# Kernel tuning notes

Measured on AMD Instinct MI355X. Metric: run time of the kernel, lower is better.

The kernel has to match this reference:

```python
import jax, jax.numpy as jnp
import numpy as np

D_MODEL = 1024
NUM_HEADS = 16
D_K = D_MODEL // NUM_HEADS


def setup_inputs() -> dict:
    key = jax.random.key(0)
    ks = jax.random.split(key, 9)
    B, S = 2, 2048
    scale = 1.0 / np.sqrt(D_MODEL)
    x = jax.random.normal(ks[0], (B, S, D_MODEL), dtype=jnp.float32)
    Wq = jax.random.normal(ks[1], (D_MODEL, D_MODEL), dtype=jnp.float32) * scale
    Wk = jax.random.normal(ks[2], (D_MODEL, D_MODEL), dtype=jnp.float32) * scale
    Wv = jax.random.normal(ks[3], (D_MODEL, D_MODEL), dtype=jnp.float32) * scale
    Wo = jax.random.normal(ks[4], (D_MODEL, D_MODEL), dtype=jnp.float32) * scale
    bq = jax.random.normal(ks[5], (D_MODEL,), dtype=jnp.float32) * 0.01
    bk = jax.random.normal(ks[6], (D_MODEL,), dtype=jnp.float32) * 0.01
    bv = jax.random.normal(ks[7], (D_MODEL,), dtype=jnp.float32) * 0.01
    bo = jax.random.normal(ks[8], (D_MODEL,), dtype=jnp.float32) * 0.01
    return {"x": x, "Wq": Wq, "bq": bq, "Wk": Wk, "bk": bk,
            "Wv": Wv, "bv": bv, "Wo": Wo, "bo": bo}


def reference(x, Wq, bq, Wk, bk, Wv, bv, Wo, bo):
    B, S, _ = x.shape
    H, Dk = NUM_HEADS, D_K
    # projections -> [B, H, S, Dk]
    def split_heads(t):
        return t.reshape(B, S, H, Dk).transpose(0, 2, 1, 3)
    q = split_heads(x @ Wq + bq)
    k = split_heads(x @ Wk + bk)
    v = split_heads(x @ Wv + bv)
    # full score matrix [B, H, S, S] (faithful to the original non-fused impl)
    scores = jnp.einsum('bhqd,bhkd->bhqk', q, k) / jnp.sqrt(jnp.float32(Dk))
    attn = jax.nn.softmax(scores, axis=-1)
    out = jnp.einsum('bhqk,bhkd->bhqd', attn, v)
    out = out.transpose(0, 2, 1, 3).reshape(B, S, H * Dk)
    return out @ Wo + bo
```

## Files before the change

### kernel.cpp

```cpp
#include <hip/hip_runtime.h>
#include <cstdint>

constexpr int S    = 2048;
constexpr int D    = 1024;
constexpr int NH   = 16;
constexpr int DK   = 64;
constexpr int MTOK = 2 * S;

typedef __bf16 bf16x8 __attribute__((ext_vector_type(8)));
typedef __bf16 bf16x4 __attribute__((ext_vector_type(4)));
typedef float  floatx4 __attribute__((ext_vector_type(4)));
typedef unsigned uintx4 __attribute__((ext_vector_type(4)));

__device__ __forceinline__ void async_cp16(const void* g, void* l) {
    __builtin_amdgcn_global_load_lds(
        (const __attribute__((address_space(1))) uint32_t*)g,
        (__attribute__((address_space(3))) uint32_t*)l, 16, 0, 0);
}

__device__ __forceinline__ void swap_rows32(unsigned &a, unsigned &b) {
#if __has_builtin(__builtin_amdgcn_permlane32_swap)
    typedef unsigned u32x2 __attribute__((ext_vector_type(2)));
    u32x2 r = __builtin_amdgcn_permlane32_swap(a, b, false, false);
    a = r[0]; b = r[1];
#else
    asm volatile("v_permlane32_swap_b32 %0, %1" : "+v"(a), "+v"(b));
#endif
}
__device__ __forceinline__ void swap_rows16(unsigned &a, unsigned &b) {
#if __has_builtin(__builtin_amdgcn_permlane16_swap)
    typedef unsigned u32x2 __attribute__((ext_vector_type(2)));
    u32x2 r = __builtin_amdgcn_permlane16_swap(a, b, false, false);
    a = r[0]; b = r[1];
#else
    asm volatile("v_permlane16_swap_b32 %0, %1" : "+v"(a), "+v"(b));
#endif
}

__global__ __launch_bounds__(256) void cvt_prep(
    const float* __restrict__ x, __bf16* __restrict__ xb,
    const float* __restrict__ W0, const float* __restrict__ W1,
    const float* __restrict__ W2, const float* __restrict__ W3,
    __bf16* __restrict__ T0, __bf16* __restrict__ T1,
    __bf16* __restrict__ T2, __bf16* __restrict__ T3)
{
    const int t = threadIdx.x;
    if (blockIdx.z == 4) {
        int blk = blockIdx.y * 16 + blockIdx.x;
        const float4* src = (const float4*)x;
        #pragma unroll
        for (int ii = 0; ii < 16; ++ii) {
            int idx = blk * 4096 + ii * 256 + t;
            float4 v = src[idx];
            bf16x4 o;
            o[0] = (__bf16)v.x; o[1] = (__bf16)v.y; o[2] = (__bf16)v.z; o[3] = (__bf16)v.w;
            *(bf16x4*)&xb[(size_t)idx * 4] = o;
        }
        return;
    }
    const float* W = (blockIdx.z == 0) ? W0 : (blockIdx.z == 1) ? W1 : (blockIdx.z == 2) ? W2 : W3;
    __bf16*      T = (blockIdx.z == 0) ? T0 : (blockIdx.z == 1) ? T1 : (blockIdx.z == 2) ? T2 : T3;
    __shared__ __bf16 tile[64][65];
    const int k0 = blockIdx.y * 64, n0 = blockIdx.x * 64;
    #pragma unroll
    for (int i = 0; i < 4; ++i) {
        int k = (t >> 4) + i * 16;
        int n = (t & 15) * 4;
        float4 v = *(const float4*)&W[(size_t)(k0 + k) * D + n0 + n];
        tile[n + 0][k] = (__bf16)v.x;
        tile[n + 1][k] = (__bf16)v.y;
        tile[n + 2][k] = (__bf16)v.z;
        tile[n + 3][k] = (__bf16)v.w;
    }
    __syncthreads();
    #pragma unroll
    for (int i = 0; i < 4; ++i) {
        int n = (t >> 4) + i * 16;
        int k = (t & 15) * 4;
        bf16x4 o;
        o[0] = tile[n][k]; o[1] = tile[n][k + 1]; o[2] = tile[n][k + 2]; o[3] = tile[n][k + 3];
        *(bf16x4*)&T[(size_t)(n0 + n) * D + k0 + k] = o;
    }
}

constexpr int BM = 128, BK = 64;

template<int JT>
__device__ __forceinline__ void gemm_core(
    const __bf16* __restrict__ A, const __bf16* __restrict__ Bt,
    __bf16* Alds, __bf16* Blds, int m0, int n0, floatx4 (&acc)[4][JT])
{
    const int tid = threadIdx.x;
    const int w = tid >> 6, l = tid & 63;
    const int wm = (w >> 1) * 64, wn = (w & 1) * 16 * JT;
    const int lr = l & 15, lg = l >> 4;

    #pragma unroll
    for (int i = 0; i < 4; ++i)
        #pragma unroll
        for (int j = 0; j < JT; ++j)
            acc[i][j] = (floatx4){0.f, 0.f, 0.f, 0.f};

    for (int k0 = 0; k0 < D; k0 += BK) {
        #pragma unroll
        for (int i = 0; i < 4; ++i) {
            int c = i * 256 + tid, row = c >> 3, g = c & 7;
            async_cp16(&A[(size_t)(m0 + row) * D + k0 + g * 8], &Alds[c * 8]);
        }
        #pragma unroll
        for (int i = 0; i < JT; ++i) {
            int c = i * 256 + tid, row = c >> 3, g = c & 7;
            async_cp16(&Bt[(size_t)(n0 + row) * D + k0 + g * 8], &Blds[c * 8]);
        }
        __syncthreads();
        #pragma unroll
        for (int kk = 0; kk < 2; ++kk) {
            bf16x8 af[4], bfr[JT];
            #pragma unroll
            for (int i = 0; i < 4; ++i)
                af[i] = *(const bf16x8*)&Alds[(wm + i * 16 + lr) * BK + kk * 32 + lg * 8];
            #pragma unroll
            for (int j = 0; j < JT; ++j)
                bfr[j] = *(const bf16x8*)&Blds[(wn + j * 16 + lr) * BK + kk * 32 + lg * 8];
            #pragma unroll
            for (int i = 0; i < 4; ++i)
                #pragma unroll
                for (int j = 0; j < JT; ++j)
                    acc[i][j] = __builtin_amdgcn_mfma_f32_16x16x32_bf16(af[i], bfr[j], acc[i][j], 0, 0, 0);
        }
        __syncthreads();
    }
}

__global__ __launch_bounds__(256, 2) void gemm_qkv(
    const __bf16* __restrict__ xb,
    const __bf16* __restrict__ WqT, const __bf16* __restrict__ WkT, const __bf16* __restrict__ WvT,
    const float* __restrict__ bq, const float* __restrict__ bk, const float* __restrict__ bv,
    __bf16* __restrict__ Qb, __bf16* __restrict__ Kb, __bf16* __restrict__ Vt)
{
    __shared__ __align__(16) __bf16 Alds[BM * BK];
    __shared__ __align__(16) __bf16 Blds[128 * BK];
    const int z = blockIdx.z;
    const __bf16* Bt   = (z == 0) ? WqT : (z == 1) ? WkT : WvT;
    const float*  bias = (z == 0) ? bq : (z == 1) ? bk : bv;
    const float   scale = (z == 0) ? 0.18033688f : 1.0f;
    const int m0 = blockIdx.y * BM, n0 = blockIdx.x * 128;

    floatx4 acc[4][4];
    gemm_core<4>(xb, Bt, Alds, Blds, m0, n0, acc);

    const int tid = threadIdx.x;
    const int w = tid >> 6, l = tid & 63;
    const int wm = (w >> 1) * 64, wn = (w & 1) * 64;
    const int lr = l & 15, lg = l >> 4;

    if (z < 2) {
        __bf16* Out = (z == 0) ? Qb : Kb;
        #pragma unroll
        for (int i = 0; i < 4; ++i)
            #pragma unroll
            for (int j = 0; j < 4; ++j) {
                int n = n0 + wn + j * 16 + lr;
                #pragma unroll
                for (int r = 0; r < 4; ++r) {
                    int m = m0 + wm + i * 16 + lg * 4 + r;
                    float v = (acc[i][j][r] + bias[n]) * scale;
                    size_t off = ((size_t)((m >> 11) * NH + (n >> 6)) * S + (m & (S - 1))) * DK + (n & (DK - 1));
                    Out[off] = (__bf16)v;
                }
            }
    } else {
        #pragma unroll
        for (int i = 0; i < 4; ++i)
            #pragma unroll
            for (int j = 0; j < 4; ++j) {
                int n = n0 + wn + j * 16 + lr;
                int m = m0 + wm + i * 16 + lg * 4;
                float bn = bias[n];
                bf16x4 o;
                #pragma unroll
                for (int r = 0; r < 4; ++r) o[r] = (__bf16)(acc[i][j][r] + bn);
                size_t off = ((size_t)((m >> 11) * NH + (n >> 6)) * DK + (n & (DK - 1))) * S + (m & (S - 1));
                *(bf16x4*)&Vt[off] = o;
            }
    }
}

__global__ __launch_bounds__(256, 2) void gemm_out(
    const __bf16* __restrict__ A, const __bf16* __restrict__ Bt,
    const float* __restrict__ bias, float* __restrict__ Cout)
{
    __shared__ __align__(16) __bf16 Alds[BM * BK];
    __shared__ __align__(16) __bf16 Blds[64 * BK];
    const int m0 = blockIdx.y * BM, n0 = blockIdx.x * 64;

    floatx4 acc[4][2];
    gemm_core<2>(A, Bt, Alds, Blds, m0, n0, acc);

    const int tid = threadIdx.x;
    const int w = tid >> 6, l = tid & 63;
    const int wm = (w >> 1) * 64, wn = (w & 1) * 32;
    const int lr = l & 15, lg = l >> 4;
    #pragma unroll
    for (int i = 0; i < 4; ++i)
        #pragma unroll
        for (int j = 0; j < 2; ++j) {
            int n = n0 + wn + j * 16 + lr;
            #pragma unroll
            for (int r = 0; r < 4; ++r) {
                int m = m0 + wm + i * 16 + lg * 4 + r;
                Cout[(size_t)m * D + n] = acc[i][j][r] + bias[n];
            }
        }
}

constexpr int QT = 128;
constexpr int KT = 64;
constexpr float SOFTMAX_C2 = 14.4269504f;

__device__ __forceinline__ unsigned pkexp(float a, float b) {
    __bf16 lo = (__bf16)__builtin_amdgcn_exp2f(a - SOFTMAX_C2);
    __bf16 hi = (__bf16)__builtin_amdgcn_exp2f(b - SOFTMAX_C2);
    unsigned ls = (unsigned)__builtin_bit_cast(unsigned short, lo);
    unsigned hs = (unsigned)__builtin_bit_cast(unsigned short, hi);
    return ls | (hs << 16);
}

__global__ __launch_bounds__(256, 2) void attn_mfma(
    const __bf16* __restrict__ Q, const __bf16* __restrict__ K,
    const __bf16* __restrict__ Vt, __bf16* __restrict__ O)
{
    __shared__ __align__(16) __bf16 Klds[2][KT * DK];
    __shared__ __align__(16) __bf16 Vlds[2][DK * KT];

    const int tid = threadIdx.x;
    const int w = tid >> 6, l = tid & 63;
    const int lr = l & 15, lg = l >> 4;
    const int sw = lr & 7;
    const int bh = blockIdx.y;
    const int q0 = blockIdx.x * QT;
    const __bf16* Kbase = K  + (size_t)bh * S * DK;
    const __bf16* Vbase = Vt + (size_t)bh * DK * S;

    bf16x8 qf[2][2];
    {
        const __bf16* qp = Q + ((size_t)bh * S + q0 + w * 32) * DK;
        #pragma unroll
        for (int i = 0; i < 2; ++i)
            #pragma unroll
            for (int kk = 0; kk < 2; ++kk)
                qf[i][kk] = *(const bf16x8*)&qp[(i * 16 + lr) * DK + kk * 32 + lg * 8];
    }
    bf16x8 vones;
    #pragma unroll
    for (int j = 0; j < 8; ++j) vones[j] = (__bf16)1.0f;

    floatx4 acc[4][2];
    #pragma unroll
    for (int jd = 0; jd < 4; ++jd)
        #pragma unroll
        for (int i = 0; i < 2; ++i)
            acc[jd][i] = (floatx4){0.f, 0.f, 0.f, 0.f};
    floatx4 psacc[2];
    psacc[0] = (floatx4){0.f, 0.f, 0.f, 0.f};
    psacc[1] = (floatx4){0.f, 0.f, 0.f, 0.f};

    bf16x8 kreg[2], vreg[2];
    auto gload = [&](int t0) {
        #pragma unroll
        for (int ii = 0; ii < 2; ++ii) {
            int c = ii * 256 + tid, row = c >> 3, g = c & 7;
            kreg[ii] = *(const bf16x8*)&Kbase[(size_t)(t0 + row) * DK + g * 8];
            vreg[ii] = *(const bf16x8*)&Vbase[(size_t)row * S + t0 + g * 8];
        }
    };
    auto lwrite = [&](int buf) {
        #pragma unroll
        for (int ii = 0; ii < 2; ++ii) {
            int c = ii * 256 + tid, row = c >> 3, gs = (c & 7) ^ (row & 7);
            *(bf16x8*)&Klds[buf][row * 64 + gs * 8] = kreg[ii];
            *(bf16x8*)&Vlds[buf][row * 64 + gs * 8] = vreg[ii];
        }
    };

    gload(0);
    lwrite(0);
    gload(KT);

    for (int t0 = 0; t0 < S; t0 += KT) {
        const int cur = (t0 >> 6) & 1;
        __syncthreads();

        floatx4 sa[4][2];
        #pragma unroll
        for (int j = 0; j < 4; ++j)
            #pragma unroll
            for (int i = 0; i < 2; ++i)
                sa[j][i] = (floatx4){0.f, 0.f, 0.f, 0.f};
        #pragma unroll
        for (int kk = 0; kk < 2; ++kk) {
            bf16x8 kf[4];
            #pragma unroll
            for (int j = 0; j < 4; ++j)
                kf[j] = *(const bf16x8*)&Klds[cur][(j * 16 + lr) * DK + (((kk * 4 + lg) ^ sw) * 8)];
            #pragma unroll
            for (int j = 0; j < 4; ++j)
                #pragma unroll
                for (int i = 0; i < 2; ++i)
                    sa[j][i] = __builtin_amdgcn_mfma_f32_16x16x32_bf16(kf[j], qf[i][kk], sa[j][i], 0, 0, 0);
        }

        bf16x8 pfr[2][2];
        #pragma unroll
        for (int i = 0; i < 2; ++i)
            #pragma unroll
            for (int kk = 0; kk < 2; ++kk) {
                const int j0 = kk * 2, j1 = j0 + 1;
                unsigned pa = pkexp(sa[j0][i][0], sa[j0][i][1]);
                unsigned pc = pkexp(sa[j0][i][2], sa[j0][i][3]);
                unsigned pb = pkexp(sa[j1][i][0], sa[j1][i][1]);
                unsigned pd = pkexp(sa[j1][i][2], sa[j1][i][3]);
                swap_rows32(pa, pb); swap_rows16(pa, pb);
                swap_rows32(pc, pd); swap_rows16(pc, pd);
                uintx4 pw = {pa, pc, pb, pd};
                pfr[kk][i] = __builtin_bit_cast(bf16x8, pw);
            }

        #pragma unroll
        for (int kk = 0; kk < 2; ++kk) {
            bf16x8 vf[4];
            #pragma unroll
            for (int jd = 0; jd < 4; ++jd)
                vf[jd] = *(const bf16x8*)&Vlds[cur][(jd * 16 + lr) * KT + (((kk * 4 + lg) ^ sw) * 8)];
            #pragma unroll
            for (int jd = 0; jd < 4; ++jd)
                #pragma unroll
                for (int i = 0; i < 2; ++i)
                    acc[jd][i] = __builtin_amdgcn_mfma_f32_16x16x32_bf16(vf[jd], pfr[kk][i], acc[jd][i], 0, 0, 0);
            #pragma unroll
            for (int i = 0; i < 2; ++i)
                psacc[i] = __builtin_amdgcn_mfma_f32_16x16x32_bf16(vones, pfr[kk][i], psacc[i], 0, 0, 0);
        }

        if (t0 + KT < S) {
            lwrite(cur ^ 1);
            if (t0 + 2 * KT < S) gload(t0 + 2 * KT);
        }
    }

    const int b = bh >> 4, h = bh & 15;
    #pragma unroll
    for (int i = 0; i < 2; ++i) {
        float inv = 1.f / psacc[i][0];
        int q = q0 + w * 32 + i * 16 + lr;
        __bf16* op = O + (size_t)(b * S + q) * D + h * DK;
        #pragma unroll
        for (int jd = 0; jd < 4; ++jd) {
            bf16x4 ov;
            #pragma unroll
            for (int r = 0; r < 4; ++r) ov[r] = (__bf16)(acc[jd][i][r] * inv);
            *(bf16x4*)&op[jd * 16 + lg * 4] = ov;
        }
    }
}

extern "C" void kernel_launch(void* const* d_in, const int* in_sizes, int n_in,
                              void* d_out, int out_size, void* d_ws, size_t ws_size,
                              hipStream_t stream) {
    const float* x  = (const float*)d_in[0];
    const float* Wq = (const float*)d_in[1];
    const float* bq = (const float*)d_in[2];
    const float* Wk = (const float*)d_in[3];
    const float* bk = (const float*)d_in[4];
    const float* Wv = (const float*)d_in[5];
    const float* bv = (const float*)d_in[6];
    const float* Wo = (const float*)d_in[7];
    const float* bo = (const float*)d_in[8];

    char* ws = (char*)d_ws;
    __bf16* xb  = (__bf16*)(ws);
    __bf16* WqT = (__bf16*)(ws + (8ull  << 20));
    __bf16* WkT = (__bf16*)(ws + (10ull << 20));
    __bf16* WvT = (__bf16*)(ws + (12ull << 20));
    __bf16* WoT = (__bf16*)(ws + (14ull << 20));
    __bf16* Qb  = (__bf16*)(ws + (16ull << 20));
    __bf16* Kb  = (__bf16*)(ws + (24ull << 20));
    __bf16* Vt  = (__bf16*)(ws + (32ull << 20));
    __bf16* Ob  = (__bf16*)(ws + (40ull << 20));

    cvt_prep<<<dim3(16, 16, 5), 256, 0, stream>>>(
        x, xb, Wq, Wk, Wv, Wo, WqT, WkT, WvT, WoT);

    gemm_qkv<<<dim3(D / 128, MTOK / BM, 3), 256, 0, stream>>>(
        xb, WqT, WkT, WvT, bq, bk, bv, Qb, Kb, Vt);

    attn_mfma<<<dim3(S / QT, 2 * NH), 256, 0, stream>>>(Qb, Kb, Vt, Ob);

    gemm_out<<<dim3(D / 64, MTOK / BM), 256, 0, stream>>>(Ob, WoT, bo, (float*)d_out);
}
```

Measured before the change: 193.9 us.

## Load K/V fragments directly from global into registers, dropping LDS staging

The attention kernel no longer stages K and V tiles through double-buffered shared memory with barriers. Each wave now loads its MFMA fragments straight from global memory, prefetching the next K tile into a ping-pong register set while V is loaded per step. The softmax offset is folded into the score accumulator's initial value, packing uses v_cvt_pk_bf16_f32, and s_setprio raises priority around the MFMA blocks. This removes the LDS writes and __syncthreads, but the four waves in a block now each read the same K/V tile from global or cache, which raises memory traffic and register pressure.

```diff
diff --git a/kernel.cpp b/kernel.cpp
--- a/kernel.cpp
+++ b/kernel.cpp
@@ -218,25 +218,21 @@
 constexpr int KT = 64;
 constexpr float SOFTMAX_C2 = 14.4269504f;
 
-__device__ __forceinline__ unsigned pkexp(float a, float b) {
-    __bf16 lo = (__bf16)__builtin_amdgcn_exp2f(a - SOFTMAX_C2);
-    __bf16 hi = (__bf16)__builtin_amdgcn_exp2f(b - SOFTMAX_C2);
-    unsigned ls = (unsigned)__builtin_bit_cast(unsigned short, lo);
-    unsigned hs = (unsigned)__builtin_bit_cast(unsigned short, hi);
-    return ls | (hs << 16);
+__device__ __forceinline__ unsigned pkexp2(float a, float b) {
+    float lo = __builtin_amdgcn_exp2f(a);
+    float hi = __builtin_amdgcn_exp2f(b);
+    unsigned r;
+    asm("v_cvt_pk_bf16_f32 %0, %1, %2" : "=v"(r) : "v"(lo), "v"(hi));
+    return r;
 }
 
 __global__ __launch_bounds__(256, 2) void attn_mfma(
     const __bf16* __restrict__ Q, const __bf16* __restrict__ K,
     const __bf16* __restrict__ Vt, __bf16* __restrict__ O)
 {
-    __shared__ __align__(16) __bf16 Klds[2][KT * DK];
-    __shared__ __align__(16) __bf16 Vlds[2][DK * KT];
-
     const int tid = threadIdx.x;
     const int w = tid >> 6, l = tid & 63;
     const int lr = l & 15, lg = l >> 4;
-    const int sw = lr & 7;
     const int bh = blockIdx.y;
     const int q0 = blockIdx.x * QT;
     const __bf16* Kbase = K  + (size_t)bh * S * DK;
@@ -265,50 +261,37 @@
     psacc[0] = (floatx4){0.f, 0.f, 0.f, 0.f};
     psacc[1] = (floatx4){0.f, 0.f, 0.f, 0.f};
 
-    bf16x8 kreg[2], vreg[2];
-    auto gload = [&](int t0) {
-        #pragma unroll
-        for (int ii = 0; ii < 2; ++ii) {
-            int c = ii * 256 + tid, row = c >> 3, g = c & 7;
-            kreg[ii] = *(const bf16x8*)&Kbase[(size_t)(t0 + row) * DK + g * 8];
-            vreg[ii] = *(const bf16x8*)&Vbase[(size_t)row * S + t0 + g * 8];
-        }
+    auto loadK = [&](bf16x8 (&kf)[2][4], int t0) {
+        #pragma unroll
+        for (int kk = 0; kk < 2; ++kk)
+            #pragma unroll
+            for (int j = 0; j < 4; ++j)
+                kf[kk][j] = *(const bf16x8*)&Kbase[(size_t)(t0 + j * 16 + lr) * DK + kk * 32 + lg * 8];
     };
-    auto lwrite = [&](int buf) {
-        #pragma unroll
-        for (int ii = 0; ii < 2; ++ii) {
-            int c = ii * 256 + tid, row = c >> 3, gs = (c & 7) ^ (row & 7);
-            *(bf16x8*)&Klds[buf][row * 64 + gs * 8] = kreg[ii];
-            *(bf16x8*)&Vlds[buf][row * 64 + gs * 8] = vreg[ii];
-        }
-    };
-
-    gload(0);
-    lwrite(0);
-    gload(KT);
-
-    for (int t0 = 0; t0 < S; t0 += KT) {
-        const int cur = (t0 >> 6) & 1;
-        __syncthreads();
+
+    auto step = [&](bf16x8 (&kcur)[2][4], bf16x8 (&knxt)[2][4], int t0) {
+        bf16x8 vf[2][4];
+        #pragma unroll
+        for (int kk = 0; kk < 2; ++kk)
+            #pragma unroll
+            for (int jd = 0; jd < 4; ++jd)
+                vf[kk][jd] = *(const bf16x8*)&Vbase[(size_t)(jd * 16 + lr) * S + t0 + kk * 32 + lg * 8];
 
         floatx4 sa[4][2];
         #pragma unroll
         for (int j = 0; j < 4; ++j)
             #pragma unroll
             for (int i = 0; i < 2; ++i)
-                sa[j][i] = (floatx4){0.f, 0.f, 0.f, 0.f};
-        #pragma unroll
-        for (int kk = 0; kk < 2; ++kk) {
-            bf16x8 kf[4];
+                sa[j][i] = (floatx4){-SOFTMAX_C2, -SOFTMAX_C2, -SOFTMAX_C2, -SOFTMAX_C2};
+        __builtin_amdgcn_s_setprio(1);
+        #pragma unroll
+        for (int kk = 0; kk < 2; ++kk)
             #pragma unroll
             for (int j = 0; j < 4; ++j)
-                kf[j] = *(const bf16x8*)&Klds[cur][(j * 16 + lr) * DK + (((kk * 4 + lg) ^ sw) * 8)];
-            #pragma unroll
-            for (int j = 0; j < 4; ++j)
                 #pragma unroll
                 for (int i = 0; i < 2; ++i)
-                    sa[j][i] = __builtin_amdgcn_mfma_f32_16x16x32_bf16(kf[j], qf[i][kk], sa[j][i], 0, 0, 0);
-        }
+                    sa[j][i] = __builtin_amdgcn_mfma_f32_16x16x32_bf16(kcur[kk][j], qf[i][kk], sa[j][i], 0, 0, 0);
+        __builtin_amdgcn_s_setprio(0);
 
         bf16x8 pfr[2][2];
         #pragma unroll
@@ -316,36 +299,38 @@
             #pragma unroll
             for (int kk = 0; kk < 2; ++kk) {
                 const int j0 = kk * 2, j1 = j0 + 1;
-                unsigned pa = pkexp(sa[j0][i][0], sa[j0][i][1]);
-                unsigned pc = pkexp(sa[j0][i][2], sa[j0][i][3]);
-                unsigned pb = pkexp(sa[j1][i][0], sa[j1][i][1]);
-                unsigned pd = pkexp(sa[j1][i][2], sa[j1][i][3]);
+                unsigned pa = pkexp2(sa[j0][i][0], sa[j0][i][1]);
+                unsigned pc = pkexp2(sa[j0][i][2], sa[j0][i][3]);
+                unsigned pb = pkexp2(sa[j1][i][0], sa[j1][i][1]);
+                unsigned pd = pkexp2(sa[j1][i][2], sa[j1][i][3]);
                 swap_rows32(pa, pb); swap_rows16(pa, pb);
                 swap_rows32(pc, pd); swap_rows16(pc, pd);
                 uintx4 pw = {pa, pc, pb, pd};
                 pfr[kk][i] = __builtin_bit_cast(bf16x8, pw);
             }
 
+        if (t0 + KT < S) loadK(knxt, t0 + KT);
+
+        __builtin_amdgcn_s_setprio(1);
         #pragma unroll
         for (int kk = 0; kk < 2; ++kk) {
-            bf16x8 vf[4];
             #pragma unroll
             for (int jd = 0; jd < 4; ++jd)
-                vf[jd] = *(const bf16x8*)&Vlds[cur][(jd * 16 + lr) * KT + (((kk * 4 + lg) ^ sw) * 8)];
-            #pragma unroll
-            for (int jd = 0; jd < 4; ++jd)
                 #pragma unroll
                 for (int i = 0; i < 2; ++i)
-                    acc[jd][i] = __builtin_amdgcn_mfma_f32_16x16x32_bf16(vf[jd], pfr[kk][i], acc[jd][i], 0, 0, 0);
+                    acc[jd][i] = __builtin_amdgcn_mfma_f32_16x16x32_bf16(vf[kk][jd], pfr[kk][i], acc[jd][i], 0, 0, 0);
             #pragma unroll
             for (int i = 0; i < 2; ++i)
                 psacc[i] = __builtin_amdgcn_mfma_f32_16x16x32_bf16(vones, pfr[kk][i], psacc[i], 0, 0, 0);
         }
-
-        if (t0 + KT < S) {
-            lwrite(cur ^ 1);
-            if (t0 + 2 * KT < S) gload(t0 + 2 * KT);
-        }
+        __builtin_amdgcn_s_setprio(0);
+    };
+
+    bf16x8 kfA[2][4], kfB[2][4];
+    loadK(kfA, 0);
+    for (int t0 = 0; t0 < S; t0 += 2 * KT) {
+        step(kfA, kfB, t0);
+        step(kfB, kfA, t0 + KT);
     }
 
     const int b = bh >> 4, h = bh & 15;
```

Result: slower. 262.0 us (+35.1%).
